# Optimization experiments

Measured on AMD Instinct MI355X. Metric: run time of the kernel, lower is better.

Reference implementation:

```python
import jax, jax.numpy as jnp
import numpy as np

D_IN, D_MODEL, N_STATE, N_LAYERS, N_CLASSES = 64, 256, 32, 4, 10
B, S = 8, 8192
EPS = 1e-8


def rmsnorm(x, scale):
    # norm = ||x||_2 / sqrt(d); y = scale * x / (norm + eps)
    norm = jnp.linalg.norm(x, axis=-1, keepdims=True) / np.sqrt(x.shape[-1])
    return scale * x / (norm + EPS)


def ssm_layer(h, log_A, Bw, Bb, Cw, Cb):
    # h: [B,S,d]; diagonal linear recurrence h_t = A*h_{t-1} + B@x_t, y_t = C@h_t
    A = jax.nn.sigmoid(log_A)                      # [n]
    bx = jnp.einsum('bsd,nd->bsn', h, Bw) + Bb     # [B,S,n]

    def step(carry, bx_t):
        carry = A * carry + bx_t                   # [B,n]
        return carry, carry

    h0 = jnp.zeros((h.shape[0], N_STATE), dtype=h.dtype)
    _, hs = jax.lax.scan(step, h0, jnp.swapaxes(bx, 0, 1))  # hs: [S,B,n]
    hs = jnp.swapaxes(hs, 0, 1)                    # [B,S,n]
    return jnp.einsum('bsn,dn->bsd', hs, Cw) + Cb  # [B,S,d]


def setup_inputs() -> dict:
    key = jax.random.key(0)
    ks = jax.random.split(key, 16)
    sc = 0.02
    return {
        'x': jax.random.normal(ks[0], (B, S, D_IN), dtype=jnp.float32),
        'in_w': jax.random.normal(ks[1], (D_MODEL, D_IN), dtype=jnp.float32) * sc,
        'in_b': jnp.zeros((D_MODEL,), dtype=jnp.float32),
        'log_A': jax.random.normal(ks[2], (N_LAYERS, N_STATE), dtype=jnp.float32) * 0.1 - 1.0,
        'Bw': jax.random.normal(ks[3], (N_LAYERS, N_STATE, D_MODEL), dtype=jnp.float32) * sc,
        'Bb': jnp.zeros((N_LAYERS, N_STATE), dtype=jnp.float32),
        'Cw': jax.random.normal(ks[4], (N_LAYERS, D_MODEL, N_STATE), dtype=jnp.float32) * sc,
        'Cb': jnp.zeros((N_LAYERS, D_MODEL), dtype=jnp.float32),
        'norm_scale': jnp.ones((N_LAYERS, D_MODEL), dtype=jnp.float32),
        'fn_scale': jnp.ones((D_MODEL,), dtype=jnp.float32),
        'cl_w1': jax.random.normal(ks[5], (D_MODEL, D_MODEL), dtype=jnp.float32) * sc,
        'cl_b1': jnp.zeros((D_MODEL,), dtype=jnp.float32),
        'cl_w2': jax.random.normal(ks[6], (N_CLASSES, D_MODEL), dtype=jnp.float32) * sc,
        'cl_b2': jnp.zeros((N_CLASSES,), dtype=jnp.float32),
    }


def reference(x, in_w, in_b, log_A, Bw, Bb, Cw, Cb, norm_scale, fn_scale,
              cl_w1, cl_b1, cl_w2, cl_b2):
    h = jnp.einsum('bsi,di->bsd', x, in_w) + in_b  # input_proj (dropout=identity in eval)
    for l in range(N_LAYERS):
        residual = h
        hn = rmsnorm(h, norm_scale[l])
        hn = ssm_layer(hn, log_A[l], Bw[l], Bb[l], Cw[l], Cb[l])
        h = hn + residual
    h = rmsnorm(h, fn_scale)
    h = h.mean(axis=1)                              # [B,d]
    h1 = jax.nn.silu(jnp.einsum('bd,ed->be', h, cl_w1) + cl_b1)
    logits = jnp.einsum('bd,cd->bc', h1, cl_w2) + cl_b2
    return logits
```

## Files before the change

### kernel.cpp

```cpp
#include <hip/hip_runtime.h>
#include <hip/hip_fp16.h>
#include <math.h>

#define B_    8
#define S_    8192
#define DIN   64
#define DM    256
#define NS    32
#define NL    4
#define TOUT  128
#define NWARM 64
#define PIPE  192
#define HIST  16
#define NBLK  512
#define NTHR  384

#define OFF_G   0
#define OFF_GX  4096
#define OFF_G0  4160
#define OFF_WY  4224
#define OFF_WU  12416
#define OFF_P   20608
#define OFF_R   26752
#define OFF_CY  36992
#define OFF_CU  37120
#define OFF_TX  37248
#define OFF_TV  37504
#define OFF_CT  37824
#define OFF_CC  37828
#define OFF_AV  37832
#define PRE_N   37960

#define TXOFF  18432
#define TVOFF  18560
#define WS_FRAG 40960
#define WS_PART 65536
#define WS_XP   165888

#define LX    0
#define LS0   6528
#define LNQ   19584
#define LTL   19776
#define LDSN  19968

typedef _Float16 h2_t  __attribute__((ext_vector_type(2)));
typedef _Float16 f16x8 __attribute__((ext_vector_type(8)));
typedef float    f32x4 __attribute__((ext_vector_type(4)));
typedef uint     uv4   __attribute__((ext_vector_type(4)));

__device__ __forceinline__ float h2f(ushort u) { return __half2float(__ushort_as_half(u)); }
__device__ __forceinline__ ushort f2h(float f) { return __half_as_ushort(__float2half(f)); }
__device__ __forceinline__ uint pack2(float a, float b) {
  return (uint)f2h(a) | ((uint)f2h(b) << 16);
}
__device__ __forceinline__ float fdot2h(uint w, uint v, float c) {
  return __builtin_amdgcn_fdot2(__builtin_bit_cast(h2_t, w),
                                __builtin_bit_cast(h2_t, v), c, false);
}
__device__ __forceinline__ f32x4 MF(uv4 a, uv4 b, f32x4 c) {
  return __builtin_amdgcn_mfma_f32_16x16x32_f16(
      __builtin_bit_cast(f16x8, a), __builtin_bit_cast(f16x8, b), c, 0, 0, 0);
}
__device__ __forceinline__ uv4 ldB(const uint* __restrict__ Fr, int unit, int lane) {
  return ((const uv4*)Fr)[unit * 64 + lane];
}

__global__ void ssm_xpose(const float* __restrict__ in_w, const float* __restrict__ Cw,
                          const float* __restrict__ in_b, const float* __restrict__ Cb,
                          float* __restrict__ xp)
{
  const int g = blockIdx.x * 256 + threadIdx.x;
  if (g < 64 * 256) {
    const int i = g >> 8, d = g & 255;
    xp[g] = in_w[d * 64 + i];
  } else if (g < 64 * 256 + 128 * 256) {
    const int r = g - 64 * 256, ln = r >> 8, d = r & 255;
    const int l = ln >> 5, n = ln & 31;
    xp[16384 + r] = Cw[(l * DM + d) * NS + n];
  } else if (g < 64 * 256 + 128 * 256 + 4 * 256) {
    const int r = g - (64 * 256 + 128 * 256), l = r >> 8, d = r & 255;
    float bs = in_b[d];
    for (int lp = 0; lp < l; ++lp) bs += Cb[lp * DM + d];
    xp[49152 + r] = bs;
  }
}

__global__ __launch_bounds__(256) void ssm_prep(
    const float* __restrict__ logA, const float* __restrict__ Bw,
    const float* __restrict__ nsc, const float* __restrict__ in_b,
    const float* __restrict__ Cb, const float* __restrict__ xp,
    float* __restrict__ Wf, ushort* __restrict__ FrH)
{
  const int t = blockIdx.x * 4 + (threadIdx.x >> 6);
  const int lane = threadIdx.x & 63;
  if (t >= PRE_N) return;
  const int pm6[6]  = {1,2,2,3,3,3}, pl6[6] = {0,0,1,0,1,2};
  const int rm10[10] = {0,1,1,2,2,2,3,3,3,3}, rl10[10] = {0,0,1,0,1,2,0,1,2,3};
  const float* in_wT = xp;
  const float* CwT   = xp + 16384;
  const float* bsT   = xp + 49152;

  const float* pa = nullptr;
  const float* pb = nullptr;
  const float* pn = nullptr;
  float s = 0.f;
  if (t < OFF_GX) {
    pa = in_wT + (t >> 6) * 256; pb = in_wT + (t & 63) * 256;
  } else if (t < OFF_G0) {
    pa = in_wT + (t - OFF_GX) * 256; pb = in_b;
  } else if (t < OFF_WY) {
    if (t == OFF_G0) { pa = in_b; pb = in_b; }
  } else if (t < OFF_WU) {
    const int r = t - OFF_WY, l = r >> 11, qq = r & 2047, c = qq >> 5, n = qq & 31;
    pa = Bw + (l*NS + n)*DM; pn = nsc + l*DM; pb = in_wT + c*256;
  } else if (t < OFF_P) {
    const int r = t - OFF_WU, l = r >> 11, qq = r & 2047, c = qq >> 5, n = qq & 31;
    pa = CwT + (l*32 + n)*256; pb = in_wT + c*256;
  } else if (t < OFF_R) {
    const int r = t - OFF_P, pi = r >> 10, qq = r & 1023, np = qq >> 5, n = qq & 31;
    const int m = pm6[pi], lp = pl6[pi];
    pa = Bw + (m*NS + n)*DM; pn = nsc + m*DM; pb = CwT + (lp*32 + np)*256;
  } else if (t < OFF_CY) {
    const int r = t - OFF_R, ri = r >> 10, qq = r & 1023, np = qq >> 5, n = qq & 31;
    const int m = rm10[ri], lp = rl10[ri];
    pa = CwT + (m*32 + n)*256; pb = CwT + (lp*32 + np)*256;
  } else if (t < OFF_CU) {
    const int r = t - OFF_CY, l = r >> 5, n = r & 31;
    pa = Bw + (l*NS + n)*DM; pn = nsc + l*DM; pb = bsT + l*256;
  } else if (t < OFF_TX) {
    const int r = t - OFF_CU, l = r >> 5, n = r & 31;
    pa = CwT + (l*32 + n)*256; pb = bsT + l*256;
  } else if (t < OFF_TV) {
    const int r = t - OFF_TX, l = r >> 6, i = r & 63;
    pa = Cb + l*DM; pb = in_wT + i*256;
  } else if (t < OFF_CT) {
    const int r = t - OFF_TV, vi = r >> 5, np = r & 31;
    const int m = rm10[vi], lp = rl10[vi];
    pa = Cb + m*DM; pb = CwT + (lp*32 + np)*256;
  } else if (t < OFF_CC) {
    const int l = t - OFF_CT;
    pa = Cb + l*DM; pb = bsT + l*256;
  } else if (t < OFF_AV) {
    const int l = t - OFF_CC;
    pa = Cb + l*DM; pb = Cb + l*DM;
  } else {
    if (lane == 0) s = 1.0f / (1.0f + expf(-logA[t - OFF_AV]));
  }
  if (pa) {
    float4 va = ((const float4*)pa)[lane];
    const float4 vb = ((const float4*)pb)[lane];
    if (pn) {
      const float4 vn = ((const float4*)pn)[lane];
      va.x *= vn.x; va.y *= vn.y; va.z *= vn.z; va.w *= vn.w;
    }
    s = fmaf(va.x, vb.x, fmaf(va.y, vb.y, fmaf(va.z, vb.z, va.w * vb.w)));
  }
  #pragma unroll
  for (int off = 1; off < 64; off <<= 1) s += __shfl_xor(s, off, 64);
  if (lane != 0) return;
  Wf[t] = s;

  if (t < OFF_GX) {
    const int kk = t >> 6, n = t & 63;
    const int u = (kk >> 5)*4 + (n >> 4);
    const int ln2 = (((kk & 31) >> 3) << 4) + (n & 15);
    FrH[(u*256 + ln2*4 + ((kk & 7) >> 1))*2 + (kk & 1)] = f2h(s);
  } else if (t >= OFF_WY && t < OFF_WU) {
    const int r = t - OFF_WY, l = r >> 11, kk = (r & 2047) >> 5, n = r & 31;
    const int u = 8 + l*4 + (kk >> 5)*2 + (n >> 4);
    const int ln2 = (((kk & 31) >> 3) << 4) + (n & 15);
    FrH[(u*256 + ln2*4 + ((kk & 7) >> 1))*2 + (kk & 1)] = f2h(s);
  } else if (t >= OFF_WU && t < OFF_P) {
    const int r = t - OFF_WU, l = r >> 11, kk = (r & 2047) >> 5, n = r & 31;
    const int u = 24 + l*4 + (kk >> 5)*2 + (n >> 4);
    const int ln2 = (((kk & 31) >> 3) << 4) + (n & 15);
    FrH[(u*256 + ln2*4 + ((kk & 7) >> 1))*2 + (kk & 1)] = f2h(s);
  } else if (t >= OFF_P && t < OFF_R) {
    const int r = t - OFF_P, pi = r >> 10, kk = (r & 1023) >> 5, n = r & 31;
    const int u = 40 + pi*2 + (n >> 4);
    const int ln2 = ((kk >> 3) << 4) + (n & 15);
    FrH[(u*256 + ln2*4 + ((kk & 7) >> 1))*2 + (kk & 1)] = f2h(s);
  } else if (t >= OFF_R && t < OFF_CY) {
    const int r = t - OFF_R, ri = r >> 10, kk = (r & 1023) >> 5, n = r & 31;
    const int u = 52 + ri*2 + (n >> 4);
    const int ln2 = ((kk >> 3) << 4) + (n & 15);
    const float sc = (ri == 0 || ri == 2 || ri == 5 || ri == 9) ? 0.5f : 1.f;
    FrH[(u*256 + ln2*4 + ((kk & 7) >> 1))*2 + (kk & 1)] = f2h(s * sc);
  } else if (t >= OFF_TX && t < OFF_TV) {
    const int r = t - OFF_TX, l = r >> 6, i = r & 63;
    FrH[(TXOFF + l*32 + (i >> 1))*2 + (i & 1)] = f2h(s);
  } else if (t >= OFF_TV && t < OFF_CT) {
    const int r = t - OFF_TV, vi = r >> 5, nn = r & 31;
    FrH[(TVOFF + vi*16 + (nn >> 1))*2 + (nn & 1)] = f2h(s);
  }
}

template<int L>
__device__ __forceinline__ void layer_mfma(
    const int tid, const int lane, const int wid, const int s0base,
    uint* lds, const float* __restrict__ Wf, const uint* __restrict__ Fr,
    const float* __restrict__ Bb,
    const uv4 (&xf)[2][2], uv4 (&sf0)[2], uv4 (&sf1)[2], uv4 (&sf2)[2], uv4 (&sf3)[2])
{
  constexpr int RB = L * (L + 1) / 2;
  constexpr int PB = (L == 1) ? 0 : (L == 2) ? 1 : 3;
  constexpr int SL = LS0 + L * 3264;
  float*  ldsF = (float*)lds;
  ushort* ldsH = (ushort*)lds;
  const int li = lane & 15, q4 = (lane >> 4) & 3;

  float cy[2], bb2[2], cu[2], tvs[2];
  #pragma unroll
  for (int nt = 0; nt < 2; ++nt) {
    const int nn = nt*16 + li;
    cy[nt]  = Wf[OFF_CY + L*32 + nn];
    bb2[nt] = Bb[L*32 + nn];
    cu[nt]  = Wf[OFF_CU + L*32 + nn];
    tvs[nt] = Wf[OFF_TV + (RB + L)*32 + nn];
  }
  float invv[2][4];
  #pragma unroll
  for (int m = 0; m < 2; ++m)
    #pragma unroll
    for (int r = 0; r < 4; ++r) {
      const int tk = wid*32 + m*16 + q4*4 + r;
      invv[m][r] = 1.0f / (sqrtf(fmaxf(ldsF[LNQ + tk], 0.f)) * 0.0625f + 1e-8f);
    }

  #pragma unroll
  for (int nt = 0; nt < 2; ++nt) {
    const uv4 by0 = ldB(Fr, 8 + L*4 + 0*2 + nt, lane);
    const uv4 by1 = ldB(Fr, 8 + L*4 + 1*2 + nt, lane);
    uv4 bp0, bp1, bp2;
    if constexpr (L > 0) bp0 = ldB(Fr, 40 + (PB + 0)*2 + nt, lane);
    if constexpr (L > 1) bp1 = ldB(Fr, 40 + (PB + 1)*2 + nt, lane);
    if constexpr (L > 2) bp2 = ldB(Fr, 40 + (PB + 2)*2 + nt, lane);
    #pragma unroll
    for (int m = 0; m < 2; ++m) {
      f32x4 c = {cy[nt], cy[nt], cy[nt], cy[nt]};
      c = MF(xf[m][0], by0, c);
      c = MF(xf[m][1], by1, c);
      if constexpr (L > 0) c = MF(sf0[m], bp0, c);
      if constexpr (L > 1) c = MF(sf1[m], bp1, c);
      if constexpr (L > 2) c = MF(sf2[m], bp2, c);
      #pragma unroll
      for (int r = 0; r < 4; ++r) {
        const int tk = wid*32 + m*16 + q4*4 + r;
        const bool valid = (s0base > 0) || (tk >= NWARM);
        const float v = valid ? fmaf(invv[m][r], c[r], bb2[nt]) : 0.f;
        ldsH[SL*2 + tk*34 + nt*16 + li] = f2h(v);
      }
    }
  }
  __syncthreads();

  const int n = tid & 31, g = tid >> 5;
  const float a = Wf[OFF_AV + L*32 + n];
  float dv[HIST + 16];
  #pragma unroll
  for (int k = 0; k < HIST + 16; ++k) {
    const int p = g*16 - HIST + k;
    dv[k] = (p >= 0) ? h2f(ldsH[SL*2 + p*34 + n]) : 0.f;
  }
  __syncthreads();

  {
    float carry = 0.f;
    #pragma unroll
    for (int k = 0; k < HIST + 16; ++k) {
      carry = fmaf(a, carry, dv[k]);
      if (k >= HIST) ldsH[SL*2 + (g*16 + k - HIST)*34 + n] = f2h(carry);
    }
  }
  if (tid < PIPE) {
    float tl = Wf[OFF_CT + L];
    const uint* xr = lds + LX + tid*34;
    #pragma unroll 8
    for (int c2 = 0; c2 < 32; ++c2) tl = fdot2h(Fr[TXOFF + L*32 + c2], xr[c2], tl);
    if constexpr (L > 0) { const uint* sr = lds + LS0 + 0*3264 + tid*17;
      #pragma unroll
      for (int m2 = 0; m2 < 16; ++m2) tl = fdot2h(Fr[TVOFF + (RB+0)*16 + m2], sr[m2], tl); }
    if constexpr (L > 1) { const uint* sr = lds + LS0 + 1*3264 + tid*17;
      #pragma unroll
      for (int m2 = 0; m2 < 16; ++m2) tl = fdot2h(Fr[TVOFF + (RB+1)*16 + m2], sr[m2], tl); }
    if constexpr (L > 2) { const uint* sr = lds + LS0 + 2*3264 + tid*17;
      #pragma unroll
      for (int m2 = 0; m2 < 16; ++m2) tl = fdot2h(Fr[TVOFF + (RB+2)*16 + m2], sr[m2], tl); }
    ldsF[LTL + tid] = tl;
  }
  __syncthreads();

  uv4 sA[2];
  #pragma unroll
  for (int m = 0; m < 2; ++m) {
    const uint* p = lds + SL + (wid*32 + m*16 + li)*17 + q4*4;
    uv4 v; v[0] = p[0]; v[1] = p[1]; v[2] = p[2]; v[3] = p[3];
    sA[m] = v;
  }
  if constexpr (L == 0)      { sf0[0] = sA[0]; sf0[1] = sA[1]; }
  else if constexpr (L == 1) { sf1[0] = sA[0]; sf1[1] = sA[1]; }
  else if constexpr (L == 2) { sf2[0] = sA[0]; sf2[1] = sA[1]; }
  else                       { sf3[0] = sA[0]; sf3[1] = sA[1]; }

  float wv[2][4] = {{0,0,0,0},{0,0,0,0}};
  #pragma unroll
  for (int nt = 0; nt < 2; ++nt) {
    const uv4 bu0 = ldB(Fr, 24 + L*4 + 0*2 + nt, lane);
    const uv4 bu1 = ldB(Fr, 24 + L*4 + 1*2 + nt, lane);
    uv4 br0, br1, br2;
    if constexpr (L > 0) br0 = ldB(Fr, 52 + (RB + 0)*2 + nt, lane);
    if constexpr (L > 1) br1 = ldB(Fr, 52 + (RB + 1)*2 + nt, lane);
    if constexpr (L > 2) br2 = ldB(Fr, 52 + (RB + 2)*2 + nt, lane);
    const uv4 brS = ldB(Fr, 52 + (RB + L)*2 + nt, lane);
    #pragma unroll
    for (int m = 0; m < 2; ++m) {
      f32x4 c = {0.f, 0.f, 0.f, 0.f};
      c = MF(xf[m][0], bu0, c);
      c = MF(xf[m][1], bu1, c);
      if constexpr (L > 0) c = MF(sf0[m], br0, c);
      if constexpr (L > 1) c = MF(sf1[m], br1, c);
      if constexpr (L > 2) c = MF(sf2[m], br2, c);
      c = MF(sA[m], brS, c);
      #pragma unroll
      for (int r = 0; r < 4; ++r) {
        const int tk = wid*32 + m*16 + q4*4 + r;
        const float sv = h2f(ldsH[SL*2 + tk*34 + nt*16 + li]);
        wv[m][r] = fmaf(c[r] + cu[nt] + tvs[nt], sv, wv[m][r]);
      }
    }
  }
  #pragma unroll
  for (int m = 0; m < 2; ++m)
    #pragma unroll
    for (int r = 0; r < 4; ++r) {
      float v = wv[m][r];
      v += __shfl_xor(v, 1, 64); v += __shfl_xor(v, 2, 64);
      v += __shfl_xor(v, 4, 64); v += __shfl_xor(v, 8, 64);
      wv[m][r] = v;
    }
  if (li == 0) {
    #pragma unroll
    for (int m = 0; m < 2; ++m)
      #pragma unroll
      for (int r = 0; r < 4; ++r) {
        const int tk = wid*32 + m*16 + q4*4 + r;
        ldsF[LNQ + tk] += 2.f * (wv[m][r] + ldsF[LTL + tk]);
      }
  }
  __syncthreads();
}

__global__ __launch_bounds__(NTHR, 2) void ssm_main(
    const float* __restrict__ x, const float* __restrict__ Wf,
    const uint* __restrict__ Fr, const float* __restrict__ Bb,
    float* __restrict__ part)
{
  extern __shared__ uint lds[];
  float*  ldsF = (float*)lds;
  ushort* ldsH = (ushort*)lds;
  const int tid = threadIdx.x;
  const int lane = tid & 63, wid = tid >> 6;
  const int li = lane & 15, q4 = (lane >> 4) & 3;
  const int blk = blockIdx.x;
  const int bb = blk >> 6;
  const int s0base = (blk & 63) * TOUT;

  {
    const float4* xg4 = (const float4*)(x + (size_t)bb * S_ * DIN);
    #pragma unroll
    for (int k = 0; k < 8; ++k) {
      const int idx = k * NTHR + tid;
      const int tok = idx >> 4, c4 = idx & 15;
      const int lt = s0base - NWARM + tok;
      float4 v = make_float4(0.f, 0.f, 0.f, 0.f);
      if (lt >= 0) v = xg4[lt * 16 + c4];
      lds[LX + tok*34 + 2*c4]     = pack2(v.x, v.y);
      lds[LX + tok*34 + 2*c4 + 1] = pack2(v.z, v.w);
    }
  }
  __syncthreads();

  uv4 xf[2][2];
  #pragma unroll
  for (int m = 0; m < 2; ++m)
    #pragma unroll
    for (int k = 0; k < 2; ++k) {
      const uint* p = lds + LX + (wid*32 + m*16 + li)*34 + k*16 + q4*4;
      uv4 v; v[0] = p[0]; v[1] = p[1]; v[2] = p[2]; v[3] = p[3];
      xf[m][k] = v;
    }

  {
    float val[2][4] = {{0,0,0,0},{0,0,0,0}};
    #pragma unroll
    for (int nt = 0; nt < 4; ++nt) {
      const float gxv = 2.f * Wf[OFF_GX + nt*16 + li];
      const uv4 bg0 = ldB(Fr, 0*4 + nt, lane);
      const uv4 bg1 = ldB(Fr, 1*4 + nt, lane);
      #pragma unroll
      for (int m = 0; m < 2; ++m) {
        f32x4 c = {gxv, gxv, gxv, gxv};
        c = MF(xf[m][0], bg0, c);
        c = MF(xf[m][1], bg1, c);
        #pragma unroll
        for (int r = 0; r < 4; ++r) {
          const int tk = wid*32 + m*16 + q4*4 + r;
          const float xv = h2f(ldsH[tk*68 + nt*16 + li]);
          val[m][r] = fmaf(c[r], xv, val[m][r]);
        }
      }
    }
    const float g0 = Wf[OFF_G0];
    #pragma unroll
    for (int m = 0; m < 2; ++m)
      #pragma unroll
      for (int r = 0; r < 4; ++r) {
        float v = val[m][r];
        v += __shfl_xor(v, 1, 64); v += __shfl_xor(v, 2, 64);
        v += __shfl_xor(v, 4, 64); v += __shfl_xor(v, 8, 64);
        if (li == 0) ldsF[LNQ + wid*32 + m*16 + q4*4 + r] = g0 + v;
      }
  }
  __syncthreads();

  uv4 sf0[2], sf1[2], sf2[2], sf3[2];
  layer_mfma<0>(tid, lane, wid, s0base, lds, Wf, Fr, Bb, xf, sf0, sf1, sf2, sf3);
  layer_mfma<1>(tid, lane, wid, s0base, lds, Wf, Fr, Bb, xf, sf0, sf1, sf2, sf3);
  layer_mfma<2>(tid, lane, wid, s0base, lds, Wf, Fr, Bb, xf, sf0, sf1, sf2, sf3);
  layer_mfma<3>(tid, lane, wid, s0base, lds, Wf, Fr, Bb, xf, sf0, sf1, sf2, sf3);

  float rr = 0.f;
  if (tid >= NWARM && tid < PIPE)
    rr = 1.0f / (sqrtf(fmaxf(ldsF[LNQ + tid], 0.f)) * 0.0625f + 1e-8f);
  const int jj = tid - NWARM;
  float* pf = (float*)lds;

  if (tid >= NWARM && tid < PIPE) {
    pf[jj*33] = rr;
    const float4* xr4 = (const float4*)(x + ((size_t)bb * S_ + (size_t)(s0base + jj)) * DIN);
    #pragma unroll
    for (int c4 = 0; c4 < 8; ++c4) {
      const float4 v = xr4[c4];
      pf[jj*33 + 1 + 4*c4] = v.x * rr; pf[jj*33 + 2 + 4*c4] = v.y * rr;
      pf[jj*33 + 3 + 4*c4] = v.z * rr; pf[jj*33 + 4 + 4*c4] = v.w * rr;
    }
  }
  __syncthreads();
  if (tid < 33) { float s = 0.f;
    for (int k = 0; k < TOUT; ++k) s += pf[k*33 + tid];
    part[blk*193 + tid] = s; }
  __syncthreads();
  if (tid >= NWARM && tid < PIPE) {
    const float4* xr4 = (const float4*)(x + ((size_t)bb * S_ + (size_t)(s0base + jj)) * DIN);
    #pragma unroll
    for (int c4 = 8; c4 < 16; ++c4) {
      const float4 v = xr4[c4];
      const int o = 4*c4 - 32;
      pf[jj*33 + o]     = v.x * rr; pf[jj*33 + o + 1] = v.y * rr;
      pf[jj*33 + o + 2] = v.z * rr; pf[jj*33 + o + 3] = v.w * rr;
    }
  }
  __syncthreads();
  if (tid < 32) { float s = 0.f;
    for (int k = 0; k < TOUT; ++k) s += pf[k*33 + tid];
    part[blk*193 + 33 + tid] = s; }
  __syncthreads();
  for (int l = 0; l < 4; ++l) {
    if (tid >= NWARM && tid < PIPE) {
      #pragma unroll
      for (int m2 = 0; m2 < 16; ++m2) {
        const uint w = lds[LS0 + l*3264 + tid*17 + m2];
        pf[jj*33 + 2*m2]     = h2f((ushort)(w & 0xffffu)) * rr;
        pf[jj*33 + 2*m2 + 1] = h2f((ushort)(w >> 16)) * rr;
      }
    }
    __syncthreads();
    if (tid < 32) { float s = 0.f;
      for (int k = 0; k < TOUT; ++k) s += pf[k*33 + tid];
      part[blk*193 + 65 + l*32 + tid] = s; }
    __syncthreads();
  }
}

__global__ __launch_bounds__(256) void ssm_final(
    const float* __restrict__ part,
    const float* __restrict__ in_w, const float* __restrict__ in_b,
    const float* __restrict__ Cw, const float* __restrict__ Cb,
    const float* __restrict__ fsc,
    const float* __restrict__ w1, const float* __restrict__ b1,
    const float* __restrict__ w2, const float* __restrict__ b2,
    float* __restrict__ out)
{
  const int b = blockIdx.x, t = threadIdx.x;
  __shared__ float red[193];
  __shared__ float meanv[DM];
  __shared__ float h1[DM];
  if (t < 193) {
    float a0 = 0.f, a1 = 0.f, a2 = 0.f, a3 = 0.f;
    const float* pp = part + (size_t)b * 64 * 193 + t;
    for (int k = 0; k < 64; k += 4) {
      a0 += pp[(k + 0) * 193]; a1 += pp[(k + 1) * 193];
      a2 += pp[(k + 2) * 193]; a3 += pp[(k + 3) * 193];
    }
    red[t] = (a0 + a1) + (a2 + a3);
  }
  __syncthreads();
  {
    const float rho = red[0];
    float m = in_b[t] * rho;
    #pragma unroll 4
    for (int i = 0; i < 64; ++i) m = fmaf(in_w[t*64 + i], red[1 + i], m);
    for (int l = 0; l < NL; ++l) {
      #pragma unroll 4
      for (int n = 0; n < 32; ++n)
        m = fmaf(Cw[(l*DM + t)*NS + n], red[65 + l*32 + n], m);
      m = fmaf(Cb[l*DM + t], rho, m);
    }
    meanv[t] = fsc[t] * m * (1.0f / (float)S_);
  }
  __syncthreads();
  {
    float z = b1[t];
    for (int e = 0; e < DM; ++e) z = fmaf(w1[t*DM + e], meanv[e], z);
    h1[t] = z / (1.0f + expf(-z));
  }
  __syncthreads();
  if (t < 10) {
    float lg = b2[t];
    for (int e = 0; e < DM; ++e) lg = fmaf(w2[t*DM + e], h1[e], lg);
    out[b*10 + t] = lg;
  }
}

extern "C" void kernel_launch(void* const* d_in, const int* in_sizes, int n_in,
                              void* d_out, int out_size, void* d_ws, size_t ws_size,
                              hipStream_t stream)
{
  const float* x    = (const float*)d_in[0];
  const float* in_w = (const float*)d_in[1];
  const float* in_b = (const float*)d_in[2];
  const float* logA = (const float*)d_in[3];
  const float* Bw   = (const float*)d_in[4];
  const float* Bb   = (const float*)d_in[5];
  const float* Cw   = (const float*)d_in[6];
  const float* Cb   = (const float*)d_in[7];
  const float* nsc  = (const float*)d_in[8];
  const float* fsc  = (const float*)d_in[9];
  const float* w1   = (const float*)d_in[10];
  const float* b1   = (const float*)d_in[11];
  const float* w2   = (const float*)d_in[12];
  const float* b2   = (const float*)d_in[13];
  float* out  = (float*)d_out;
  float* wsf  = (float*)d_ws;
  uint*  Fr   = (uint*)(wsf + WS_FRAG);
  float* part = wsf + WS_PART;
  float* xp   = wsf + WS_XP;
  (void)in_sizes; (void)n_in; (void)out_size; (void)ws_size;

  ssm_xpose<<<196, 256, 0, stream>>>(in_w, Cw, in_b, Cb, xp);
  ssm_prep<<<(PRE_N + 3) / 4, 256, 0, stream>>>(logA, Bw, nsc, in_b, Cb, xp,
                                                wsf, (ushort*)Fr);
  ssm_main<<<NBLK, NTHR, LDSN * sizeof(uint), stream>>>(x, wsf, Fr, Bb, part);
  ssm_final<<<B_, 256, 0, stream>>>(part, in_w, in_b, Cw, Cb, fsc, w1, b1, w2, b2, out);
}
```

Measured before the change: 77.65 us.

## Cut per-layer barriers by double-buffering scan input and keeping norms in registers

Each layer's pre-scan projections are written to a separate LDS slot (the next layer's state buffer, or the spent x buffer for the last layer). The scan can then read and write in place without an extra barrier between reading and writing. The running squared-norm accumulators stay in registers instead of an LDS round trip with a closing barrier, and the x-dependent tail dot products for all four layers are hoisted into one pass before the layers. This removes about two of the four block-wide barriers per layer and some redundant LDS traffic. In exchange it uses more registers and a slightly larger LDS footprint, and relies on buffer-reuse assumptions being correct.

```diff
diff --git a/kernel.cpp b/kernel.cpp
--- a/kernel.cpp
+++ b/kernel.cpp
@@ -41,7 +41,7 @@
 #define LS0   6528
 #define LNQ   19584
 #define LTL   19776
-#define LDSN  19968
+#define LDSN  20160
 
 typedef _Float16 h2_t  __attribute__((ext_vector_type(2)));
 typedef _Float16 f16x8 __attribute__((ext_vector_type(8)));
@@ -200,11 +200,13 @@
     const int tid, const int lane, const int wid, const int s0base,
     uint* lds, const float* __restrict__ Wf, const uint* __restrict__ Fr,
     const float* __restrict__ Bb,
-    const uv4 (&xf)[2][2], uv4 (&sf0)[2], uv4 (&sf1)[2], uv4 (&sf2)[2], uv4 (&sf3)[2])
+    const uv4 (&xf)[2][2], uv4 (&sf0)[2], uv4 (&sf1)[2], uv4 (&sf2)[2], uv4 (&sf3)[2],
+    float (&nq)[2][4], const float (&tlx)[4])
 {
   constexpr int RB = L * (L + 1) / 2;
   constexpr int PB = (L == 1) ? 0 : (L == 2) ? 1 : 3;
-  constexpr int SL = LS0 + L * 3264;
+  constexpr int SL   = LS0 + L * 3264;
+  constexpr int DOFF = (L < 3) ? (LS0 + (L + 1) * 3264) : LX;
   float*  ldsF = (float*)lds;
   ushort* ldsH = (ushort*)lds;
   const int li = lane & 15, q4 = (lane >> 4) & 3;
@@ -222,10 +224,8 @@
   #pragma unroll
   for (int m = 0; m < 2; ++m)
     #pragma unroll
-    for (int r = 0; r < 4; ++r) {
-      const int tk = wid*32 + m*16 + q4*4 + r;
-      invv[m][r] = 1.0f / (sqrtf(fmaxf(ldsF[LNQ + tk], 0.f)) * 0.0625f + 1e-8f);
-    }
+    for (int r = 0; r < 4; ++r)
+      invv[m][r] = 1.0f / (sqrtf(fmaxf(nq[m][r], 0.f)) * 0.0625f + 1e-8f);
 
   #pragma unroll
   for (int nt = 0; nt < 2; ++nt) {
@@ -248,35 +248,12 @@
         const int tk = wid*32 + m*16 + q4*4 + r;
         const bool valid = (s0base > 0) || (tk >= NWARM);
         const float v = valid ? fmaf(invv[m][r], c[r], bb2[nt]) : 0.f;
-        ldsH[SL*2 + tk*34 + nt*16 + li] = f2h(v);
+        ldsH[DOFF*2 + tk*34 + nt*16 + li] = f2h(v);
       }
     }
   }
-  __syncthreads();
-
-  const int n = tid & 31, g = tid >> 5;
-  const float a = Wf[OFF_AV + L*32 + n];
-  float dv[HIST + 16];
-  #pragma unroll
-  for (int k = 0; k < HIST + 16; ++k) {
-    const int p = g*16 - HIST + k;
-    dv[k] = (p >= 0) ? h2f(ldsH[SL*2 + p*34 + n]) : 0.f;
-  }
-  __syncthreads();
-
-  {
-    float carry = 0.f;
-    #pragma unroll
-    for (int k = 0; k < HIST + 16; ++k) {
-      carry = fmaf(a, carry, dv[k]);
-      if (k >= HIST) ldsH[SL*2 + (g*16 + k - HIST)*34 + n] = f2h(carry);
-    }
-  }
   if (tid < PIPE) {
-    float tl = Wf[OFF_CT + L];
-    const uint* xr = lds + LX + tid*34;
-    #pragma unroll 8
-    for (int c2 = 0; c2 < 32; ++c2) tl = fdot2h(Fr[TXOFF + L*32 + c2], xr[c2], tl);
+    float tl = Wf[OFF_CT + L] + tlx[L];
     if constexpr (L > 0) { const uint* sr = lds + LS0 + 0*3264 + tid*17;
       #pragma unroll
       for (int m2 = 0; m2 < 16; ++m2) tl = fdot2h(Fr[TVOFF + (RB+0)*16 + m2], sr[m2], tl); }
@@ -286,7 +263,21 @@
     if constexpr (L > 2) { const uint* sr = lds + LS0 + 2*3264 + tid*17;
       #pragma unroll
       for (int m2 = 0; m2 < 16; ++m2) tl = fdot2h(Fr[TVOFF + (RB+2)*16 + m2], sr[m2], tl); }
-    ldsF[LTL + tid] = tl;
+    ldsF[LTL + (L & 1)*192 + tid] = tl;
+  }
+  __syncthreads();
+
+  {
+    const int n = tid & 31, g = tid >> 5;
+    const float a = Wf[OFF_AV + L*32 + n];
+    float carry = 0.f;
+    #pragma unroll
+    for (int k = 0; k < HIST + 16; ++k) {
+      const int p = g*16 - HIST + k;
+      const float v = (p >= 0) ? h2f(ldsH[DOFF*2 + p*34 + n]) : 0.f;
+      carry = fmaf(a, carry, v);
+      if (k >= HIST) ldsH[SL*2 + (g*16 + k - HIST)*34 + n] = f2h(carry);
+    }
   }
   __syncthreads();
 
@@ -336,18 +327,9 @@
       float v = wv[m][r];
       v += __shfl_xor(v, 1, 64); v += __shfl_xor(v, 2, 64);
       v += __shfl_xor(v, 4, 64); v += __shfl_xor(v, 8, 64);
-      wv[m][r] = v;
-    }
-  if (li == 0) {
-    #pragma unroll
-    for (int m = 0; m < 2; ++m)
-      #pragma unroll
-      for (int r = 0; r < 4; ++r) {
-        const int tk = wid*32 + m*16 + q4*4 + r;
-        ldsF[LNQ + tk] += 2.f * (wv[m][r] + ldsF[LTL + tk]);
-      }
-  }
-  __syncthreads();
+      const int tk = wid*32 + m*16 + q4*4 + r;
+      nq[m][r] += 2.f * (v + ldsF[LTL + (L & 1)*192 + tk]);
+    }
 }
 
 __global__ __launch_bounds__(NTHR, 2) void ssm_main(
@@ -390,6 +372,19 @@
       xf[m][k] = v;
     }
 
+  float tlx[4] = {0.f, 0.f, 0.f, 0.f};
+  if (tid < PIPE) {
+    const uint* xr = lds + LX + tid*34;
+    #pragma unroll 8
+    for (int c2 = 0; c2 < 32; ++c2) {
+      tlx[0] = fdot2h(Fr[TXOFF + 0*32 + c2], xr[c2], tlx[0]);
+      tlx[1] = fdot2h(Fr[TXOFF + 1*32 + c2], xr[c2], tlx[1]);
+      tlx[2] = fdot2h(Fr[TXOFF + 2*32 + c2], xr[c2], tlx[2]);
+      tlx[3] = fdot2h(Fr[TXOFF + 3*32 + c2], xr[c2], tlx[3]);
+    }
+  }
+
+  float nq[2][4];
   {
     float val[2][4] = {{0,0,0,0},{0,0,0,0}};
     #pragma unroll
@@ -418,16 +413,24 @@
         float v = val[m][r];
         v += __shfl_xor(v, 1, 64); v += __shfl_xor(v, 2, 64);
         v += __shfl_xor(v, 4, 64); v += __shfl_xor(v, 8, 64);
-        if (li == 0) ldsF[LNQ + wid*32 + m*16 + q4*4 + r] = g0 + v;
+        nq[m][r] = g0 + v;
       }
   }
-  __syncthreads();
 
   uv4 sf0[2], sf1[2], sf2[2], sf3[2];
-  layer_mfma<0>(tid, lane, wid, s0base, lds, Wf, Fr, Bb, xf, sf0, sf1, sf2, sf3);
-  layer_mfma<1>(tid, lane, wid, s0base, lds, Wf, Fr, Bb, xf, sf0, sf1, sf2, sf3);
-  layer_mfma<2>(tid, lane, wid, s0base, lds, Wf, Fr, Bb, xf, sf0, sf1, sf2, sf3);
-  layer_mfma<3>(tid, lane, wid, s0base, lds, Wf, Fr, Bb, xf, sf0, sf1, sf2, sf3);
+  layer_mfma<0>(tid, lane, wid, s0base, lds, Wf, Fr, Bb, xf, sf0, sf1, sf2, sf3, nq, tlx);
+  layer_mfma<1>(tid, lane, wid, s0base, lds, Wf, Fr, Bb, xf, sf0, sf1, sf2, sf3, nq, tlx);
+  layer_mfma<2>(tid, lane, wid, s0base, lds, Wf, Fr, Bb, xf, sf0, sf1, sf2, sf3, nq, tlx);
+  layer_mfma<3>(tid, lane, wid, s0base, lds, Wf, Fr, Bb, xf, sf0, sf1, sf2, sf3, nq, tlx);
+
+  if (li == 0) {
+    #pragma unroll
+    for (int m = 0; m < 2; ++m)
+      #pragma unroll
+      for (int r = 0; r < 4; ++r)
+        ldsF[LNQ + wid*32 + m*16 + q4*4 + r] = nq[m][r];
+  }
+  __syncthreads();
 
   float rr = 0.f;
   if (tid >= NWARM && tid < PIPE)
```

Result: slower. 91.91 us (+18.4%).
